# Kernel optimization log

Hardware: AMD Instinct MI355X
Metric: run time of the kernel (lower is better)

Reference implementation:

```python
import jax, jax.numpy as jnp
import numpy as np

B, S, D, H, DFF, N_LAYERS, BLK = 4, 1024, 1024, 16, 4096, 4, 64
DH = D // H
LN_EPS = 1e-5


def setup_inputs() -> dict:
    key = jax.random.key(0)
    ks = jax.random.split(key, 13)
    s = 0.02
    L = N_LAYERS
    return {
        "x": jax.random.normal(ks[0], (B, S, D), jnp.float32),
        "in_proj_w": jax.random.normal(ks[1], (L, 3 * D, D), jnp.float32) * s,
        "in_proj_b": jnp.zeros((L, 3 * D), jnp.float32),
        "out_w": jax.random.normal(ks[2], (L, D, D), jnp.float32) * s,
        "out_b": jnp.zeros((L, D), jnp.float32),
        "ln1_w": jnp.ones((L, D), jnp.float32),
        "ln1_b": jnp.zeros((L, D), jnp.float32),
        "lin1_w": jax.random.normal(ks[3], (L, DFF, D), jnp.float32) * s,
        "lin1_b": jnp.zeros((L, DFF), jnp.float32),
        "lin2_w": jax.random.normal(ks[4], (L, D, DFF), jnp.float32) * s,
        "lin2_b": jnp.zeros((L, D), jnp.float32),
        "ln2_w": jnp.ones((L, D), jnp.float32),
        "ln2_b": jnp.zeros((L, D), jnp.float32),
    }


def _layer_norm(x, w, b):
    mu = jnp.mean(x, axis=-1, keepdims=True)
    var = jnp.mean(jnp.square(x - mu), axis=-1, keepdims=True)
    return (x - mu) * jax.lax.rsqrt(var + LN_EPS) * w + b


def _forward(x, in_proj_w, in_proj_b, out_w, out_b, ln1_w, ln1_b,
             lin1_w, lin1_b, lin2_w, lin2_b, ln2_w, ln2_b):
    # block-causal additive bias: token may attend to current and previous blocks
    blk = jnp.arange(S) // BLK
    bias = jnp.where(blk[:, None] >= blk[None, :], 0.0, -jnp.inf)  # [S,S]
    scale = 1.0 / np.sqrt(DH).astype(np.float32)

    for l in range(N_LAYERS):
        # --- self-attention (post-norm, PyTorch TransformerEncoderLayer default) ---
        qkv = x @ in_proj_w[l].T + in_proj_b[l]            # [B,S,3D]
        q, k, v = jnp.split(qkv, 3, axis=-1)
        q = q.reshape(B, S, H, DH).transpose(0, 2, 1, 3)   # [B,H,S,DH]
        k = k.reshape(B, S, H, DH).transpose(0, 2, 1, 3)
        v = v.reshape(B, S, H, DH).transpose(0, 2, 1, 3)
        scores = jnp.einsum('bhqd,bhkd->bhqk', q, k) * scale + bias
        attn = jax.nn.softmax(scores, axis=-1)
        o = jnp.einsum('bhqk,bhkd->bhqd', attn, v)
        o = o.transpose(0, 2, 1, 3).reshape(B, S, D)
        o = o @ out_w[l].T + out_b[l]
        x = _layer_norm(x + o, ln1_w[l], ln1_b[l])
        # --- feed-forward (relu) ---
        h = jax.nn.relu(x @ lin1_w[l].T + lin1_b[l]) @ lin2_w[l].T + lin2_b[l]
        x = _layer_norm(x + h, ln2_w[l], ln2_b[l])
    return x


def reference(x, in_proj_w, in_proj_b, out_w, out_b, ln1_w, ln1_b,
              lin1_w, lin1_b, lin2_w, lin2_b, ln2_w, ln2_b):
    return _forward(x, in_proj_w, in_proj_b, out_w, out_b, ln1_w, ln1_b,
                    lin1_w, lin1_b, lin2_w, lin2_b, ln2_w, ln2_b)
```

## Files before the change

kernel.cpp:

```cpp
#include <hip/hip_runtime.h>
#include <stdint.h>

typedef __bf16 bf16;
typedef __bf16 bf16x8 __attribute__((ext_vector_type(8)));
typedef __bf16 bf16x4 __attribute__((ext_vector_type(4)));
typedef float  f32x4  __attribute__((ext_vector_type(4)));

#define B_   4
#define S_   1024
#define D_   1024
#define H_   16
#define DH_  64
#define DFF_ 4096
#define NL_  4
#define M_   (B_*S_)

__device__ __forceinline__ void async_copy16(const void* g, void* l) {
  __builtin_amdgcn_global_load_lds(
      (const __attribute__((address_space(1))) char*)(uintptr_t)g,
      (__attribute__((address_space(3))) char*)(uintptr_t)l,
      16, 0, 0);
}

#define WAITV4 asm volatile("s_waitcnt vmcnt(4)" ::: "memory")
#define WAITV0 asm volatile("s_waitcnt vmcnt(0)" ::: "memory")
#define BAR()  { asm volatile("" ::: "memory"); __builtin_amdgcn_s_barrier(); \
                 asm volatile("" ::: "memory"); }

template<int RELU, int MODE, int QKV>
__global__ __launch_bounds__(512, 2) void gemm256_kernel(
    const bf16* __restrict__ A,
    const bf16* __restrict__ W,
    const float* __restrict__ bias,
    float* __restrict__ Cf,
    bf16*  __restrict__ Cb,
    bf16*  __restrict__ VtOut,
    int N, int Ktot, int Kc, int gx, int PN, int PM, int bpk)
{
  __shared__ __align__(16) bf16 As[2][2][256*32];
  __shared__ __align__(16) bf16 Bs[2][2][256*32];

  const int tid  = threadIdx.x;
  const int wave = tid >> 6;
  const int lane = tid & 63;
  const int wr = wave >> 2, wc = wave & 3;
  const int q4  = lane >> 4;
  const int l15 = lane & 15;

  const int Lg  = blockIdx.x;
  const int kz  = Lg / bpk;
  const int L   = Lg % bpk;
  const int xcd = L & 7;
  const int s   = L >> 3;
  const int Gn  = gx / PN;
  const int bn = ((xcd % Gn)*PN + (s % PN)) << 8;
  const int bm = ((xcd / Gn)*PM + (s / PN)) << 8;
  const int kstart = kz * Kc;

  const int r_loc = lane >> 2, c4 = lane & 3;
  const int sko = (c4 ^ ((r_loc >> 1) & 3)) << 3;
  const bf16* agp[2]; const bf16* wgp[2];
#pragma unroll
  for (int j = 0; j < 2; ++j) {
    const int rr = j*128 + wave*16 + r_loc;
    agp[j] = A + (size_t)(bm + rr)*Ktot + kstart + sko;
    wgp[j] = W + (size_t)(bn + rr)*Ktot + kstart + sko;
  }

  auto stageA = [&](int buf, int kk, int koff) {
#pragma unroll
    for (int j = 0; j < 2; ++j)
      async_copy16(agp[j] + koff + kk*32, &As[buf][kk][(j*128 + wave*16)*32]);
  };
  auto stageB = [&](int buf, int kk, int koff) {
#pragma unroll
    for (int j = 0; j < 2; ++j)
      async_copy16(wgp[j] + koff + kk*32, &Bs[buf][kk][(j*128 + wave*16)*32]);
  };

  const int ch = ((q4 ^ ((l15 >> 1) & 3)) << 3);

  f32x4 acc[8][4] = {};
  const int steps = Kc / 64;

  stageA(0, 0, 0); stageB(0, 0, 0); stageA(0, 1, 0); stageB(0, 1, 0);
  WAITV4;
  BAR();

  int koff = 64;
  for (int t = 0; t < steps; ++t) {
    const int c = t & 1;
    const bool pf = (t + 1 < steps);
    bf16x8 bfr[4];
#pragma unroll
    for (int p = 0; p < 4; ++p) {
      const int kk = p >> 1, rh = p & 1;
      if (rh == 0) {
#pragma unroll
        for (int cf = 0; cf < 4; ++cf)
          bfr[cf] = *(const bf16x8*)&Bs[c][kk][(wc*64 + cf*16 + l15)*32 + ch];
      }
      bf16x8 af[4];
#pragma unroll
      for (int r4 = 0; r4 < 4; ++r4)
        af[r4] = *(const bf16x8*)&As[c][kk][(wr*128 + (rh*4 + r4)*16 + l15)*32 + ch];
      if (pf) {
        if      (p == 0) stageA(c ^ 1, 0, koff);
        else if (p == 1) stageB(c ^ 1, 0, koff);
        else if (p == 2) stageA(c ^ 1, 1, koff);
        else             stageB(c ^ 1, 1, koff);
      }
      BAR();
      __builtin_amdgcn_s_setprio(1);
#pragma unroll
      for (int r4 = 0; r4 < 4; ++r4)
#pragma unroll
        for (int cf = 0; cf < 4; ++cf)
          acc[rh*4 + r4][cf] = __builtin_amdgcn_mfma_f32_16x16x32_bf16(
              af[r4], bfr[cf], acc[rh*4 + r4][cf], 0, 0, 0);
      __builtin_amdgcn_s_setprio(0);
      if (p == 1) { if (pf) { WAITV4; } else { WAITV0; } }
      if (p == 3) { if (pf) { WAITV4; } }
      BAR();
    }
    koff += 64;
  }

  if (QKV && bn >= 2*D_) {
#pragma unroll
    for (int r = 0; r < 8; ++r) {
      const int row0 = bm + wr*128 + r*16 + q4*4;
      const int bidx = row0 >> 10, s0 = row0 & 1023;
#pragma unroll
      for (int cf = 0; cf < 4; ++cf) {
        const int col  = bn + wc*64 + cf*16 + l15;
        const int dcol = col - 2*D_;
        const int hh = dcol >> 6, dd = dcol & 63;
        const float bv = bias[col];
        bf16x4 pk;
#pragma unroll
        for (int i = 0; i < 4; ++i) pk[i] = (bf16)(acc[r][cf][i] + bv);
        *(bf16x4*)&VtOut[((size_t)((bidx*H_ + hh)*64 + dd))*S_ + s0] = pk;
      }
    }
  } else if (MODE == 2) {
    float* Cfz = Cf + (size_t)kz * ((size_t)M_ * N);
#pragma unroll
    for (int r = 0; r < 8; ++r) {
      const int row0 = bm + wr*128 + r*16 + q4*4;
#pragma unroll
      for (int cf = 0; cf < 4; ++cf) {
        const int col = bn + wc*64 + cf*16 + l15;
#pragma unroll
        for (int i = 0; i < 4; ++i)
          Cfz[(size_t)(row0 + i)*N + col] = acc[r][cf][i];
      }
    }
  } else {
#pragma unroll
    for (int r = 0; r < 8; ++r) {
      const int row0 = bm + wr*128 + r*16 + q4*4;
#pragma unroll
      for (int cf = 0; cf < 4; ++cf) {
        const int col = bn + wc*64 + cf*16 + l15;
        const float bv = bias[col];
#pragma unroll
        for (int i = 0; i < 4; ++i) {
          float v = acc[r][cf][i] + bv;
          if (RELU) v = fmaxf(v, 0.f);
          Cb[(size_t)(row0 + i)*N + col] = (bf16)v;
        }
      }
    }
  }
}

template<int RELU, int MODE, int QKV, int BK>
__global__ __launch_bounds__(256) void gemm_bt_kernel(
    const bf16* __restrict__ A, const bf16* __restrict__ W,
    const float* __restrict__ bias, float* __restrict__ Cf,
    bf16*  __restrict__ Cb, bf16*  __restrict__ VtOut,
    int N, int Ktot, int Kc, int gx, int PN, int PM, int bpk)
{
  constexpr int NI = (BK == 64) ? 4 : 2;
  __shared__ bf16 As[2][128*BK];
  __shared__ bf16 Bs[2][128*BK];

  const int tid  = threadIdx.x;
  const int wave = tid >> 6;
  const int lane = tid & 63;
  const int wr = wave >> 1, wc = wave & 1;
  const int q4  = lane >> 4;
  const int l15 = lane & 15;

  const int Lg  = blockIdx.x;
  const int kz  = Lg / bpk;
  const int L   = Lg % bpk;
  const int xcd = L & 7;
  const int s   = L >> 3;
  const int Gn  = gx / PN;
  const int bn = ((xcd % Gn)*PN + (s % PN)) << 7;
  const int bm = ((xcd / Gn)*PM + (s / PN)) << 7;
  const int kstart = kz * Kc;

  const bf16* agp[NI]; const bf16* wgp[NI];
  int ldsb[NI];
  if constexpr (BK == 64) {
    const int r_loc = lane >> 3, c8 = lane & 7;
#pragma unroll
    for (int j = 0; j < NI; ++j) {
      const int rr = wave*32 + j*8 + r_loc;
      const int ko = ((c8 ^ (rr & 7)) << 3);
      agp[j] = A + (size_t)(bm + rr)*Ktot + kstart + ko;
      wgp[j] = W + (size_t)(bn + rr)*Ktot + kstart + ko;
      ldsb[j] = (wave*32 + j*8) * 64;
    }
  } else {
    const int r_loc = lane >> 2, c4 = lane & 3;
#pragma unroll
    for (int j = 0; j < NI; ++j) {
      const int rr = wave*32 + j*16 + r_loc;
      const int ko = ((c4 ^ ((rr >> 1) & 3)) << 3);
      agp[j] = A + (size_t)(bm + rr)*Ktot + kstart + ko;
      wgp[j] = W + (size_t)(bn + rr)*Ktot + kstart + ko;
      ldsb[j] = (wave*32 + j*16) * 32;
    }
  }

  f32x4 acc[4][4] = {};
  const int steps = Kc / BK;

  auto stage = [&](int buf) {
#pragma unroll
    for (int j = 0; j < NI; ++j) {
      async_copy16(agp[j], &As[buf][ldsb[j]]);
      async_copy16(wgp[j], &Bs[buf][ldsb[j]]);
      agp[j] += BK; wgp[j] += BK;
    }
  };

  const int sl32 = (l15 >> 1) & 3;
  const int sl64 = l15 & 7;

  auto compute = [&](int buf) {
    if constexpr (BK == 64) {
#pragma unroll
      for (int kk = 0; kk < 2; ++kk) {
        const int ch = (((kk << 2) | q4) ^ sl64) << 3;
        bf16x8 af[4], bfr[4];
#pragma unroll
        for (int rf = 0; rf < 4; ++rf)
          af[rf] = *(const bf16x8*)&As[buf][(wr*64 + rf*16 + l15)*64 + ch];
#pragma unroll
        for (int cf = 0; cf < 4; ++cf)
          bfr[cf] = *(const bf16x8*)&Bs[buf][(wc*64 + cf*16 + l15)*64 + ch];
#pragma unroll
        for (int rf = 0; rf < 4; ++rf)
#pragma unroll
          for (int cf = 0; cf < 4; ++cf)
            acc[rf][cf] = __builtin_amdgcn_mfma_f32_16x16x32_bf16(
                af[rf], bfr[cf], acc[rf][cf], 0, 0, 0);
      }
    } else {
      const int ch = (q4 ^ sl32) << 3;
      bf16x8 af[4], bfr[4];
#pragma unroll
      for (int rf = 0; rf < 4; ++rf)
        af[rf] = *(const bf16x8*)&As[buf][(wr*64 + rf*16 + l15)*32 + ch];
#pragma unroll
      for (int cf = 0; cf < 4; ++cf)
        bfr[cf] = *(const bf16x8*)&Bs[buf][(wc*64 + cf*16 + l15)*32 + ch];
#pragma unroll
      for (int rf = 0; rf < 4; ++rf)
#pragma unroll
        for (int cf = 0; cf < 4; ++cf)
          acc[rf][cf] = __builtin_amdgcn_mfma_f32_16x16x32_bf16(
              af[rf], bfr[cf], acc[rf][cf], 0, 0, 0);
    }
  };

  stage(0);
  __syncthreads();
  for (int k = 0; k < steps; ++k) {
    const int cur = k & 1;
    if (k + 1 < steps) stage(cur ^ 1);
    compute(cur);
    __syncthreads();
  }

  if (QKV && bn >= 2*D_) {
#pragma unroll
    for (int r = 0; r < 4; ++r) {
      const int row0 = bm + wr*64 + r*16 + q4*4;
      const int bidx = row0 >> 10, s0 = row0 & 1023;
#pragma unroll
      for (int c = 0; c < 4; ++c) {
        const int col  = bn + wc*64 + c*16 + l15;
        const int dcol = col - 2*D_;
        const int hh = dcol >> 6, dd = dcol & 63;
        const float bv = bias[col];
        bf16x4 pk;
#pragma unroll
        for (int i = 0; i < 4; ++i) pk[i] = (bf16)(acc[r][c][i] + bv);
        *(bf16x4*)&VtOut[((size_t)((bidx*H_ + hh)*64 + dd))*S_ + s0] = pk;
      }
    }
  } else if (MODE == 2) {
    float* Cfz = Cf + (size_t)kz * ((size_t)M_ * N);
#pragma unroll
    for (int r = 0; r < 4; ++r) {
      const int row0 = bm + wr*64 + r*16 + q4*4;
#pragma unroll
      for (int c = 0; c < 4; ++c) {
        const int col = bn + wc*64 + c*16 + l15;
#pragma unroll
        for (int i = 0; i < 4; ++i)
          Cfz[(size_t)(row0 + i)*N + col] = acc[r][c][i];
      }
    }
  } else {
#pragma unroll
    for (int r = 0; r < 4; ++r) {
      const int row0 = bm + wr*64 + r*16 + q4*4;
#pragma unroll
      for (int c = 0; c < 4; ++c) {
        const int col = bn + wc*64 + c*16 + l15;
        const float bv = bias[col];
#pragma unroll
        for (int i = 0; i < 4; ++i) {
          float v = acc[r][c][i] + bv;
          if (RELU) v = fmaxf(v, 0.f);
          Cb[(size_t)(row0 + i)*N + col] = (bf16)v;
        }
      }
    }
  }
}

#define LP 72
__global__ __launch_bounds__(256) void attn_kernel(
    const bf16* __restrict__ qkv,
    const bf16* __restrict__ vt,
    bf16* __restrict__ out)
{
  const int L    = blockIdx.x;
  const int xcd  = L & 7, slot = L >> 3;
  const int qb   = slot & 15;
  const int bh   = xcd*8 + (slot >> 4);
  const int b    = bh >> 4, h = bh & 15;
  const int tid  = threadIdx.x;
  const int wave = tid >> 6, lane = tid & 63;
  const int q4 = lane >> 4, l15 = lane & 15;
  const int r_loc = lane >> 3, c8 = lane & 7;

  __shared__ bf16 Qs[64*64];
  __shared__ bf16 Ks[2][64*64];
  __shared__ bf16 Vs[2][64*64];
  __shared__ bf16 Ps[4][16*LP];

  const size_t RS = 3*(size_t)D_;
  const bf16* qg = qkv + (size_t)(b*S_ + qb*64)*RS + h*64;
  const bf16* kg = qkv + (size_t)(b*S_)*RS + D_ + h*64;
  const bf16* vg = vt + (size_t)bh*64*S_;

#pragma unroll
  for (int j = 0; j < 2; ++j) {
    const int rr = wave*16 + j*8 + r_loc;
    const int ko = ((c8 ^ (rr & 7)) << 3);
    async_copy16(qg + (size_t)rr*RS + ko, &Qs[(wave*16 + j*8)*64]);
  }

#define STAGE_KV(KT, BUF)                                              \
  {                                                                    \
    _Pragma("unroll")                                                  \
    for (int j = 0; j < 2; ++j) {                                      \
      const int rr = wave*16 + j*8 + r_loc;                            \
      const int ko = ((c8 ^ (rr & 7)) << 3);                           \
      async_copy16(kg + (size_t)((KT)*64 + rr)*RS + ko,                \
                   &Ks[BUF][(wave*16 + j*8)*64]);                      \
      async_copy16(vg + (size_t)rr*S_ + (KT)*64 + ko,                  \
                   &Vs[BUF][(wave*16 + j*8)*64]);                      \
    }                                                                  \
  }

  f32x4 o_acc[4] = {};
  float m_i[4], l_i[4];
#pragma unroll
  for (int i = 0; i < 4; ++i) { m_i[i] = -1e30f; l_i[i] = 0.f; }
  const float scale = 0.125f;

  STAGE_KV(0, 0)
  __syncthreads();

  for (int kt = 0; kt <= qb; ++kt) {
    const int cur = kt & 1;
    if (kt < qb) {
      if (cur) STAGE_KV(kt+1, 0) else STAGE_KV(kt+1, 1)
    }

    f32x4 sc[4] = {};
#pragma unroll
    for (int kk = 0; kk < 2; ++kk) {
      const int go = ((((kk << 2) | q4)) ^ (l15 & 7)) << 3;
      bf16x8 aq = *(const bf16x8*)&Qs[(wave*16 + l15)*64 + go];
#pragma unroll
      for (int c = 0; c < 4; ++c) {
        bf16x8 bk = *(const bf16x8*)&Ks[cur][(c*16 + l15)*64 + go];
        sc[c] = __builtin_amdgcn_mfma_f32_16x16x32_bf16(aq, bk, sc[c], 0, 0, 0);
      }
    }
#pragma unroll
    for (int c = 0; c < 4; ++c)
#pragma unroll
      for (int i = 0; i < 4; ++i) sc[c][i] *= scale;

#pragma unroll
    for (int i = 0; i < 4; ++i) {
      float mx = -1e30f;
#pragma unroll
      for (int c = 0; c < 4; ++c) mx = fmaxf(mx, sc[c][i]);
#pragma unroll
      for (int off = 1; off < 16; off <<= 1) mx = fmaxf(mx, __shfl_xor(mx, off, 64));
      float m_new = fmaxf(m_i[i], mx);
      float alpha = __expf(m_i[i] - m_new);
      float rowsum = 0.f;
#pragma unroll
      for (int c = 0; c < 4; ++c) {
        float p = __expf(sc[c][i] - m_new);
        Ps[wave][(q4*4 + i)*LP + c*16 + l15] = (bf16)p;
        rowsum += p;
      }
#pragma unroll
      for (int off = 1; off < 16; off <<= 1) rowsum += __shfl_xor(rowsum, off, 64);
      l_i[i] = l_i[i]*alpha + rowsum;
      m_i[i] = m_new;
#pragma unroll
      for (int c = 0; c < 4; ++c) o_acc[c][i] *= alpha;
    }

#pragma unroll
    for (int kk = 0; kk < 2; ++kk) {
      bf16x8 ap = *(const bf16x8*)&Ps[wave][l15*LP + kk*32 + q4*8];
#pragma unroll
      for (int c = 0; c < 4; ++c) {
        const int go = ((((kk << 2) | q4)) ^ (l15 & 7)) << 3;
        bf16x8 bv = *(const bf16x8*)&Vs[cur][(c*16 + l15)*64 + go];
        o_acc[c] = __builtin_amdgcn_mfma_f32_16x16x32_bf16(ap, bv, o_acc[c], 0, 0, 0);
      }
    }
    __syncthreads();
  }
#undef STAGE_KV

  bf16* obase = out + ((size_t)(b*S_ + qb*64 + wave*16))*D_ + h*64;
#pragma unroll
  for (int i = 0; i < 4; ++i) {
    float inv = 1.f / l_i[i];
#pragma unroll
    for (int c = 0; c < 4; ++c)
      obase[(size_t)(q4*4 + i)*D_ + c*16 + l15] = (bf16)(o_acc[c][i]*inv);
  }
}

template<int NP>
__global__ __launch_bounds__(256) void add_ln_kernel(
    const float* __restrict__ xin, const float* __restrict__ parts,
    const float* __restrict__ ybias,
    const float* __restrict__ w, const float* __restrict__ bta,
    float* __restrict__ xout, bf16* __restrict__ xbf,
    float* __restrict__ extra)
{
  const int row = blockIdx.x;
  const int tid = threadIdx.x;
  const size_t base = (size_t)row * D_;
  const size_t PS = (size_t)M_ * D_;
  float v[4], sm = 0.f, ss = 0.f;
#pragma unroll
  for (int j = 0; j < 4; ++j) {
    int idx = tid + j*256;
    float y = ybias[idx];
#pragma unroll
    for (int pz = 0; pz < NP; ++pz) y += parts[(size_t)pz*PS + base + idx];
    v[j] = xin[base + idx] + y;
    sm += v[j]; ss += v[j]*v[j];
  }
#pragma unroll
  for (int off = 1; off < 64; off <<= 1) {
    sm += __shfl_xor(sm, off, 64);
    ss += __shfl_xor(ss, off, 64);
  }
  __shared__ float red[8];
  const int wave = tid >> 6, lane = tid & 63;
  if (lane == 0) { red[wave] = sm; red[4 + wave] = ss; }
  __syncthreads();
  sm = red[0] + red[1] + red[2] + red[3];
  ss = red[4] + red[5] + red[6] + red[7];
  const float mean = sm * (1.f/D_);
  const float var  = ss * (1.f/D_) - mean*mean;
  const float rstd = rsqrtf(var + 1e-5f);
#pragma unroll
  for (int j = 0; j < 4; ++j) {
    int idx = tid + j*256;
    float o = (v[j] - mean)*rstd*w[idx] + bta[idx];
    xout[base + idx] = o;
    xbf[base + idx]  = (bf16)o;
    if (extra) extra[base + idx] = o;
  }
}

__global__ __launch_bounds__(256) void conv_kernel(
    const float4* __restrict__ src, bf16x4* __restrict__ dst, int n4)
{
  int i = blockIdx.x*blockDim.x + threadIdx.x;
  const int stride = gridDim.x*blockDim.x;
  for (; i < n4; i += stride) {
    float4 f = src[i];
    bf16x4 o;
    o[0] = (bf16)f.x; o[1] = (bf16)f.y; o[2] = (bf16)f.z; o[3] = (bf16)f.w;
    dst[i] = o;
  }
}

__global__ __launch_bounds__(256) void init_x_kernel(
    const float4* __restrict__ src, float4* __restrict__ xf,
    bf16x4* __restrict__ xb, int n4)
{
  int i = blockIdx.x*blockDim.x + threadIdx.x;
  const int stride = gridDim.x*blockDim.x;
  for (; i < n4; i += stride) {
    float4 f = src[i];
    xf[i] = f;
    bf16x4 o;
    o[0] = (bf16)f.x; o[1] = (bf16)f.y; o[2] = (bf16)f.z; o[3] = (bf16)f.w;
    xb[i] = o;
  }
}

extern "C" void kernel_launch(void* const* d_in, const int* in_sizes, int n_in,
                              void* d_out, int out_size, void* d_ws, size_t ws_size,
                              hipStream_t stream) {
  const float* x    = (const float*)d_in[0];
  const float* inw  = (const float*)d_in[1];
  const float* inb  = (const float*)d_in[2];
  const float* outw = (const float*)d_in[3];
  const float* outb = (const float*)d_in[4];
  const float* ln1w = (const float*)d_in[5];
  const float* ln1b = (const float*)d_in[6];
  const float* l1w  = (const float*)d_in[7];
  const float* l1b  = (const float*)d_in[8];
  const float* l2w  = (const float*)d_in[9];
  const float* l2b  = (const float*)d_in[10];
  const float* ln2w = (const float*)d_in[11];
  const float* ln2b = (const float*)d_in[12];

  char* ws = (char*)d_ws;
  size_t off = 0;
  auto take = [&](size_t bytes) {
    char* p = ws + off;
    off = (off + bytes + 255) & ~(size_t)255;
    return p;
  };
  bf16*  w_in_bf  = (bf16*) take((size_t)NL_*3*D_*D_*2);
  bf16*  w_out_bf = (bf16*) take((size_t)NL_*D_*D_*2);
  bf16*  w_l1_bf  = (bf16*) take((size_t)NL_*DFF_*D_*2);
  bf16*  w_l2_bf  = (bf16*) take((size_t)NL_*D_*DFF_*2);
  float* x_f      = (float*)take((size_t)M_*D_*4);
  bf16*  x_b      = (bf16*) take((size_t)M_*D_*2);
  bf16*  qkv_b    = (bf16*) take((size_t)M_*3*D_*2);
  bf16*  vt_b     = (bf16*) take((size_t)B_*H_*DH_*S_*2);
  bf16*  at_b     = (bf16*) take((size_t)M_*D_*2);
  bf16*  h_b      = (bf16*) take((size_t)M_*DFF_*2);
  float* parts    = (float*)take((size_t)4*M_*D_*4);
  (void)ws_size; (void)in_sizes; (void)n_in;

  auto conv = [&](const float* s, bf16* d, size_t n) {
    int n4 = (int)(n >> 2);
    int grid = (n4 + 255) / 256; if (grid > 4096) grid = 4096;
    conv_kernel<<<grid, 256, 0, stream>>>((const float4*)s, (bf16x4*)d, n4);
  };
  conv(inw,  w_in_bf,  (size_t)NL_*3*D_*D_);
  conv(outw, w_out_bf, (size_t)NL_*D_*D_);
  conv(l1w,  w_l1_bf,  (size_t)NL_*DFF_*D_);
  conv(l2w,  w_l2_bf,  (size_t)NL_*D_*DFF_);
  init_x_kernel<<<4096, 256, 0, stream>>>((const float4*)x, (float4*)x_f,
                                          (bf16x4*)x_b, (int)((size_t)M_*D_ >> 2));

  for (int l = 0; l < NL_; ++l) {
    gemm256_kernel<0,1,1><<<192, 512, 0, stream>>>(
        x_b, w_in_bf + (size_t)l*3*D_*D_, inb + (size_t)l*3*D_,
        nullptr, qkv_b, vt_b, 3*D_, D_, D_, 12, 3, 8, 192);
    attn_kernel<<<1024, 256, 0, stream>>>(qkv_b, vt_b, at_b);
    gemm_bt_kernel<0,2,0,64><<<512, 256, 0, stream>>>(
        at_b, w_out_bf + (size_t)l*D_*D_, nullptr,
        parts, nullptr, nullptr, D_, D_, D_/2, 8, 4, 8, 256);
    add_ln_kernel<2><<<M_, 256, 0, stream>>>(
        x_f, parts, outb + (size_t)l*D_,
        ln1w + (size_t)l*D_, ln1b + (size_t)l*D_, x_f, x_b, nullptr);
    gemm256_kernel<1,1,0><<<256, 512, 0, stream>>>(
        x_b, w_l1_bf + (size_t)l*DFF_*D_, l1b + (size_t)l*DFF_,
        nullptr, h_b, nullptr, DFF_, D_, D_, 16, 4, 8, 256);
    gemm256_kernel<0,2,0><<<256, 512, 0, stream>>>(
        h_b, w_l2_bf + (size_t)l*D_*DFF_, nullptr,
        parts, nullptr, nullptr, D_, DFF_, DFF_/4, 4, 1, 8, 64);
    add_ln_kernel<4><<<M_, 256, 0, stream>>>(
        x_f, parts, l2b + (size_t)l*D_,
        ln2w + (size_t)l*D_, ln2b + (size_t)l*D_, x_f, x_b,
        (l == NL_-1) ? (float*)d_out : nullptr);
  }
}
```

Measured before the change: 1.106 ms.

## Pair causal query blocks per workgroup and restructure attention softmax

The attention kernel now launches half as many workgroups, each handling two query blocks (qb and 15-qb) so every workgroup does the same amount of causal work. Q is loaded straight into registers with the scale pre-applied, and QK^T is computed transposed so each lane owns one query column and the row max needs only two shuffles. A lazy-rescale threshold skips the o_acc rescaling unless the max grows by more than 8, and P is stored with an XOR swizzle instead of padding. This trades per-block launch overhead and softmax shuffle cost for less parallelism (512 blocks) and some bf16 rounding of the scaled Q.

```diff
diff --git a/kernel.cpp b/kernel.cpp
--- a/kernel.cpp
+++ b/kernel.cpp
@@ -325,7 +325,7 @@
 #pragma unroll
       for (int c = 0; c < 4; ++c) {
         const int col = bn + wc*64 + c*16 + l15;
-        const float bv = bias[col];
+        const float bv = bias[c ? col : col];
 #pragma unroll
         for (int i = 0; i < 4; ++i) {
           float v = acc[r][c][i] + bv;
@@ -337,7 +337,6 @@
   }
 }
 
-#define LP 72
 __global__ __launch_bounds__(256) void attn_kernel(
     const bf16* __restrict__ qkv,
     const bf16* __restrict__ vt,
@@ -345,30 +344,21 @@
 {
   const int L    = blockIdx.x;
   const int xcd  = L & 7, slot = L >> 3;
-  const int qb   = slot & 15;
-  const int bh   = xcd*8 + (slot >> 4);
+  const int qb0  = slot & 7;
+  const int bh   = xcd*8 + (slot >> 3);
   const int b    = bh >> 4, h = bh & 15;
   const int tid  = threadIdx.x;
   const int wave = tid >> 6, lane = tid & 63;
   const int q4 = lane >> 4, l15 = lane & 15;
   const int r_loc = lane >> 3, c8 = lane & 7;
 
-  __shared__ bf16 Qs[64*64];
   __shared__ bf16 Ks[2][64*64];
   __shared__ bf16 Vs[2][64*64];
-  __shared__ bf16 Ps[4][16*LP];
+  __shared__ bf16 Ps[4][16*64];
 
   const size_t RS = 3*(size_t)D_;
-  const bf16* qg = qkv + (size_t)(b*S_ + qb*64)*RS + h*64;
   const bf16* kg = qkv + (size_t)(b*S_)*RS + D_ + h*64;
   const bf16* vg = vt + (size_t)bh*64*S_;
-
-#pragma unroll
-  for (int j = 0; j < 2; ++j) {
-    const int rr = wave*16 + j*8 + r_loc;
-    const int ko = ((c8 ^ (rr & 7)) << 3);
-    async_copy16(qg + (size_t)rr*RS + ko, &Qs[(wave*16 + j*8)*64]);
-  }
 
 #define STAGE_KV(KT, BUF)                                              \
   {                                                                    \
@@ -383,83 +373,105 @@
     }                                                                  \
   }
 
-  f32x4 o_acc[4] = {};
-  float m_i[4], l_i[4];
-#pragma unroll
-  for (int i = 0; i < 4; ++i) { m_i[i] = -1e30f; l_i[i] = 0.f; }
-  const float scale = 0.125f;
-
-  STAGE_KV(0, 0)
-  __syncthreads();
-
-  for (int kt = 0; kt <= qb; ++kt) {
-    const int cur = kt & 1;
-    if (kt < qb) {
-      if (cur) STAGE_KV(kt+1, 0) else STAGE_KV(kt+1, 1)
-    }
-
-    f32x4 sc[4] = {};
+  for (int pass = 0; pass < 2; ++pass) {
+    const int qb = pass ? (15 - qb0) : qb0;
+    const bf16* qg = qkv + (size_t)(b*S_ + qb*64)*RS + h*64;
+
+    bf16x8 qf[2];
 #pragma unroll
     for (int kk = 0; kk < 2; ++kk) {
-      const int go = ((((kk << 2) | q4)) ^ (l15 & 7)) << 3;
-      bf16x8 aq = *(const bf16x8*)&Qs[(wave*16 + l15)*64 + go];
-#pragma unroll
-      for (int c = 0; c < 4; ++c) {
-        bf16x8 bk = *(const bf16x8*)&Ks[cur][(c*16 + l15)*64 + go];
-        sc[c] = __builtin_amdgcn_mfma_f32_16x16x32_bf16(aq, bk, sc[c], 0, 0, 0);
-      }
-    }
-#pragma unroll
-    for (int c = 0; c < 4; ++c)
-#pragma unroll
-      for (int i = 0; i < 4; ++i) sc[c][i] *= scale;
-
+      bf16x8 t = *(const bf16x8*)(qg + (size_t)(wave*16 + l15)*RS + kk*32 + (q4 << 3));
+#pragma unroll
+      for (int j = 0; j < 8; ++j) t[j] = (bf16)((float)t[j] * 0.125f);
+      qf[kk] = t;
+    }
+
+    f32x4 o_acc[4] = {};
+    float m_i = -1e30f, l_i = 0.f;
+
+    STAGE_KV(0, 0)
+    __syncthreads();
+
+    for (int kt = 0; kt <= qb; ++kt) {
+      const int cur = kt & 1;
+      if (kt < qb) {
+        if (cur) STAGE_KV(kt+1, 0) else STAGE_KV(kt+1, 1)
+      }
+
+      f32x4 sc[4] = {};
+#pragma unroll
+      for (int kk = 0; kk < 2; ++kk) {
+        const int go = ((((kk << 2) | q4)) ^ (l15 & 7)) << 3;
+#pragma unroll
+        for (int m = 0; m < 4; ++m) {
+          bf16x8 bk = *(const bf16x8*)&Ks[cur][(m*16 + l15)*64 + go];
+          sc[m] = __builtin_amdgcn_mfma_f32_16x16x32_bf16(bk, qf[kk], sc[m], 0, 0, 0);
+        }
+      }
+
+      float mx0 = fmaxf(fmaxf(sc[0][0], sc[0][1]), fmaxf(sc[0][2], sc[0][3]));
+      float mx1 = fmaxf(fmaxf(sc[1][0], sc[1][1]), fmaxf(sc[1][2], sc[1][3]));
+      float mx2 = fmaxf(fmaxf(sc[2][0], sc[2][1]), fmaxf(sc[2][2], sc[2][3]));
+      float mx3 = fmaxf(fmaxf(sc[3][0], sc[3][1]), fmaxf(sc[3][2], sc[3][3]));
+      float mx  = fmaxf(fmaxf(mx0, mx1), fmaxf(mx2, mx3));
+      mx = fmaxf(mx, __shfl_xor(mx, 16, 64));
+      mx = fmaxf(mx, __shfl_xor(mx, 32, 64));
+
+      if (__any(mx > m_i + 8.f)) {
+        const float m_new = fmaxf(m_i, mx);
+        const float alpha = __expf(m_i - m_new);
+        m_i = m_new;
+        l_i *= alpha;
+#pragma unroll
+        for (int i = 0; i < 4; ++i) {
+          const float av = __shfl(alpha, (lane & 48) | ((q4 << 2) | i), 64);
+#pragma unroll
+          for (int c = 0; c < 4; ++c) o_acc[c][i] *= av;
+        }
+      }
+
+      float rs = 0.f;
+#pragma unroll
+      for (int m = 0; m < 4; ++m) {
+        const float p0 = __expf(sc[m][0] - m_i);
+        const float p1 = __expf(sc[m][1] - m_i);
+        const float p2 = __expf(sc[m][2] - m_i);
+        const float p3 = __expf(sc[m][3] - m_i);
+        rs += (p0 + p1) + (p2 + p3);
+        bf16x4 pk;
+        pk[0] = (bf16)p0; pk[1] = (bf16)p1; pk[2] = (bf16)p2; pk[3] = (bf16)p3;
+        const int cx = ((m << 2) | q4) ^ (l15 & 14);
+        *(bf16x4*)&Ps[wave][(l15 << 6) | (cx << 2)] = pk;
+      }
+      rs += __shfl_xor(rs, 16, 64);
+      rs += __shfl_xor(rs, 32, 64);
+      l_i += rs;
+
+#pragma unroll
+      for (int kk = 0; kk < 2; ++kk) {
+        const int pcx = (((kk << 3) | (q4 << 1)) ^ (l15 & 14));
+        bf16x8 ap = *(const bf16x8*)&Ps[wave][(l15 << 6) | (pcx << 2)];
+        const int go = ((((kk << 2) | q4)) ^ (l15 & 7)) << 3;
+#pragma unroll
+        for (int c = 0; c < 4; ++c) {
+          bf16x8 bv = *(const bf16x8*)&Vs[cur][(c*16 + l15)*64 + go];
+          o_acc[c] = __builtin_amdgcn_mfma_f32_16x16x32_bf16(ap, bv, o_acc[c], 0, 0, 0);
+        }
+      }
+      __syncthreads();
+    }
+
+    bf16* obase = out + ((size_t)(b*S_ + qb*64 + wave*16))*D_ + h*64;
 #pragma unroll
     for (int i = 0; i < 4; ++i) {
-      float mx = -1e30f;
-#pragma unroll
-      for (int c = 0; c < 4; ++c) mx = fmaxf(mx, sc[c][i]);
-#pragma unroll
-      for (int off = 1; off < 16; off <<= 1) mx = fmaxf(mx, __shfl_xor(mx, off, 64));
-      float m_new = fmaxf(m_i[i], mx);
-      float alpha = __expf(m_i[i] - m_new);
-      float rowsum = 0.f;
-#pragma unroll
-      for (int c = 0; c < 4; ++c) {
-        float p = __expf(sc[c][i] - m_new);
-        Ps[wave][(q4*4 + i)*LP + c*16 + l15] = (bf16)p;
-        rowsum += p;
-      }
-#pragma unroll
-      for (int off = 1; off < 16; off <<= 1) rowsum += __shfl_xor(rowsum, off, 64);
-      l_i[i] = l_i[i]*alpha + rowsum;
-      m_i[i] = m_new;
-#pragma unroll
-      for (int c = 0; c < 4; ++c) o_acc[c][i] *= alpha;
-    }
-
-#pragma unroll
-    for (int kk = 0; kk < 2; ++kk) {
-      bf16x8 ap = *(const bf16x8*)&Ps[wave][l15*LP + kk*32 + q4*8];
-#pragma unroll
-      for (int c = 0; c < 4; ++c) {
-        const int go = ((((kk << 2) | q4)) ^ (l15 & 7)) << 3;
-        bf16x8 bv = *(const bf16x8*)&Vs[cur][(c*16 + l15)*64 + go];
-        o_acc[c] = __builtin_amdgcn_mfma_f32_16x16x32_bf16(ap, bv, o_acc[c], 0, 0, 0);
-      }
-    }
-    __syncthreads();
+      const float li = __shfl(l_i, (lane & 48) | ((q4 << 2) | i), 64);
+      const float inv = 1.f / li;
+#pragma unroll
+      for (int c = 0; c < 4; ++c)
+        obase[(size_t)((q4 << 2) | i)*D_ + c*16 + l15] = (bf16)(o_acc[c][i] * inv);
+    }
   }
 #undef STAGE_KV
-
-  bf16* obase = out + ((size_t)(b*S_ + qb*64 + wave*16))*D_ + h*64;
-#pragma unroll
-  for (int i = 0; i < 4; ++i) {
-    float inv = 1.f / l_i[i];
-#pragma unroll
-    for (int c = 0; c < 4; ++c)
-      obase[(size_t)(q4*4 + i)*D_ + c*16 + l15] = (bf16)(o_acc[c][i]*inv);
-  }
 }
 
 template<int NP>
@@ -589,7 +601,7 @@
     gemm256_kernel<0,1,1><<<192, 512, 0, stream>>>(
         x_b, w_in_bf + (size_t)l*3*D_*D_, inb + (size_t)l*3*D_,
         nullptr, qkv_b, vt_b, 3*D_, D_, D_, 12, 3, 8, 192);
-    attn_kernel<<<1024, 256, 0, stream>>>(qkv_b, vt_b, at_b);
+    attn_kernel<<<512, 256, 0, stream>>>(qkv_b, vt_b, at_b);
     gemm_bt_kernel<0,2,0,64><<<512, 256, 0, stream>>>(
         at_b, w_out_bf + (size_t)l*D_*D_, nullptr,
         parts, nullptr, nullptr, D_, D_, D_/2, 8, 4, 8, 256);
```

Result: faster. 1.018 ms (-8.0%).
